# Kernel optimization log

Measured on AMD Instinct MI355X. Metric: run time of the kernel, lower is better.

The kernel has to match this reference:

```python
import jax, jax.numpy as jnp
import numpy as np


def _conv_relu(x, w, b):
    # keras Conv2D: NHWC input, HWIO kernel, VALID padding, stride 1, relu
    y = jax.lax.conv_general_dilated(
        x, w, window_strides=(1, 1), padding='VALID',
        dimension_numbers=('NHWC', 'HWIO', 'NHWC'))
    return jax.nn.relu(y + b)


def _maxpool2(x):
    # keras MaxPooling2D((2,2)): window 2x2, stride 2, VALID
    return jax.lax.reduce_window(
        x, -jnp.inf, jax.lax.max,
        window_dimensions=(1, 2, 2, 1), window_strides=(1, 2, 2, 1),
        padding='VALID')


def setup_inputs() -> dict:
    key = jax.random.key(0)
    ks = jax.random.split(key, 8)
    B = 4096
    return {
        'x': jax.random.normal(ks[0], (B, 14, 14, 1), jnp.float32),
        'conv1_w': jax.random.normal(ks[1], (3, 3, 1, 32), jnp.float32) * 0.1,
        'conv1_b': jnp.zeros((32,), jnp.float32),
        'conv2_w': jax.random.normal(ks[2], (3, 3, 32, 64), jnp.float32) * 0.05,
        'conv2_b': jnp.zeros((64,), jnp.float32),
        # trainable grid, initialized as tf.linspace(0,1,grid_size=50)
        'grid': jnp.linspace(0.0, 1.0, 50, dtype=jnp.float32),
        # KANLayer splines: output_dim=128 weights, each (input_dim=256, grid_size=50)
        'kan1_w': jax.random.normal(ks[3], (128, 256, 50), jnp.float32) * 0.05,
        # SimplifiedKANLayer splines: output_dim=64 weights, each (input_dim=128,)
        'kan2_w': jax.random.normal(ks[4], (64, 128), jnp.float32) * 0.05,
        'dense_w': jax.random.normal(ks[5], (64, 10), jnp.float32) * 0.05,
        'dense_b': jnp.zeros((10,), jnp.float32),
    }


def reference(x, conv1_w, conv1_b, conv2_w, conv2_b, grid, kan1_w, kan2_w,
              dense_w, dense_b):
    h = _conv_relu(x, conv1_w, conv1_b)   # (B,12,12,32)
    h = _maxpool2(h)                      # (B,6,6,32)
    h = _conv_relu(h, conv2_w, conv2_b)   # (B,4,4,64)
    h = _maxpool2(h)                      # (B,2,2,64)
    B = h.shape[0]
    h = h.reshape(B, -1)                  # (B,256) keras Flatten order (H,W,C)
    # KANLayer: linear hat basis relu(1-|x-g|) per (feature,grid), contracted
    # against per-output coefficients: out[b,o] = sum_{d,g} W[o,d,g]*basis[b,d,g]
    basis = jax.nn.relu(1.0 - jnp.abs(h[:, :, None] - grid[None, None, :]))  # (B,256,50)
    h = jnp.einsum('bdg,odg->bo', basis, kan1_w)  # (B,128)
    # SimplifiedKANLayer: out[b,o] = sum_d W2[o,d]*relu(h[b,d])
    h = jnp.einsum('bd,od->bo', jax.nn.relu(h), kan2_w)  # (B,64)
    return jax.nn.softmax(h @ dense_w + dense_b, axis=-1)  # (B,10)
```

## Files before the change

### kernel.cpp

```cpp
#include <hip/hip_runtime.h>
#include <hip/hip_bf16.h>
#include <hip/hip_fp16.h>

typedef float v2f __attribute__((ext_vector_type(2)));
typedef _Float16 f16x8 __attribute__((ext_vector_type(8)));
typedef float f32x4 __attribute__((ext_vector_type(4)));

__global__ __launch_bounds__(256) void k_prep(
    const float* __restrict__ kan1_w, const float* __restrict__ w2,
    const float* __restrict__ kan2_w, __half* __restrict__ tabN,
    _Float16* __restrict__ w2f, __half2* __restrict__ w2t) {
  __shared__ float wsh[128][51];
  int bid = blockIdx.x;
  int t = threadIdx.x;
  if (bid < 256) {
    int d = bid;
#pragma unroll
    for (int i = t; i < 128 * 50; i += 256) {
      int oo = i / 50;
      int g = i - oo * 50;
      wsh[oo][g] = kan1_w[(size_t)oo * 12800 + (size_t)d * 50 + g];
    }
    __syncthreads();
    int o = t & 127;
    int jh = t >> 7;
    const float* wr = &wsh[o][0];
    __half* trow = tabN + (size_t)d * 197 * 128 + o;
    const float inv98 = 1.0f / 98.0f;
    float lowW, lowG, highW, highG;
    int k0, k1;
    if (jh == 0) {
      lowW = wr[0]; lowG = 0.f; highW = 0.f; highG = 0.f;
      for (int g = 1; g < 50; ++g) {
        highW += wr[g];
        highG += wr[g] * ((float)g * (1.0f / 49.0f));
      }
      k0 = 0; k1 = 49;
    } else {
      lowW = 0.f; lowG = 0.f; highW = 0.f; highG = 0.f;
      for (int g = 1; g < 50; ++g) {
        lowW += wr[g];
        lowG += wr[g] * ((float)g * (1.0f / 49.0f));
      }
      k0 = 49; k1 = 98;
    }
    for (int k = k0; k < k1; ++k) {
      float A = highW - lowW;
      float Bc = (lowW + highW) + lowG - highG;
      float c0 = (float)(2 * k) * inv98 + 0.5f * inv98;
      float c1 = c0 + inv98;
      trow[(size_t)(2 * k) * 128] = __float2half(fmaf(A, c0, Bc));
      trow[(size_t)(2 * k + 1) * 128] = __float2half(fmaf(A, c1, Bc));
      if (k + 1 <= 49) {
        float wg = wr[k + 1], gg = (float)(k + 1) * (1.0f / 49.0f);
        lowW += wg; lowG += wg * gg;
        highW -= wg; highG -= wg * gg;
      }
      if (k >= 48) {
        float wg = wr[k - 48], gg = (float)(k - 48) * (1.0f / 49.0f);
        lowW -= wg; lowG -= wg * gg;
      }
    }
    if (jh == 1) trow[(size_t)196 * 128] = __float2half(0.f);
    return;
  }
  if (bid < 328) {
    int i = (bid - 256) * 256 + t;
    int n = i & 63;
    int row = i >> 6;
    int ci = row & 31;
    int tap = row >> 5;
    w2f[((tap * 4 + (ci >> 3)) * 64 + n) * 8 + (ci & 7)] = (_Float16)w2[i];
    return;
  }
  {
    int i = (bid - 328) * 256 + t;
    int dp = i >> 6;
    int o = i & 63;
    w2t[i] = __floats2half2_rn(kan2_w[o * 128 + 2 * dp],
                               kan2_w[o * 128 + 2 * dp + 1]);
  }
}

#define NBC 4

__global__ __launch_bounds__(256)
__attribute__((amdgpu_waves_per_eu(2, 4))) void k_main(
    const float* __restrict__ x, const float* __restrict__ w1,
    const float* __restrict__ b1, const _Float16* __restrict__ w2f,
    const float* __restrict__ b2, const __half* __restrict__ tabN,
    const __half2* __restrict__ w2t, const float* __restrict__ dense_w,
    const float* __restrict__ dense_b, float* __restrict__ out) {
  __shared__ __align__(16) char sm1[4864];
  __shared__ __align__(16) char sm2[11520];
  float* xs = (float*)sm1;
  float* w1s = xs + NBC * 224;
  float* b1s = w1s + 288;
  unsigned short* meta = (unsigned short*)sm1;
  _Float16* h1l = (_Float16*)sm2;
  float* vs = (float*)sm2;
  float* us = vs + NBC * 128;
  float* ls = us + NBC * 64;
  int t = threadIdx.x;
  int bid = blockIdx.x;
  int b0 = bid * NBC;
  {
    for (int i = t; i < NBC * 224; i += 256) {
      int blb = i / 224;
      int rem = i - blb * 224;
      int r = rem >> 4;
      int cc = rem & 15;
      xs[i] = (cc < 14) ? x[(size_t)(b0 + blb) * 196 + r * 14 + cc] : 0.f;
    }
    for (int i = t; i < 288; i += 256) w1s[i] = w1[i];
    if (t < 32) b1s[t] = b1[t];
  }
  __syncthreads();
  int p = t >> 6;
  int c = t & 63;
  {
    int ch = c & 31;
    int half = c >> 5;
    float wr[9];
#pragma unroll
    for (int j = 0; j < 9; ++j) wr[j] = w1s[j * 32 + ch];
    float bias = b1s[ch];
    int y0 = 3 * half;
    const float* xb = xs + p * 224;
    _Float16* hrow = h1l + p * 1440 + ch;
#pragma unroll
    for (int yy = 0; yy < 3; ++yy) {
      int y = y0 + yy;
      float xr[4][16];
#pragma unroll
      for (int r = 0; r < 4; ++r) {
        float4* dstp = (float4*)xr[r];
        const float4* srcp = (const float4*)(xb + (2 * y + r) * 16);
#pragma unroll
        for (int q = 0; q < 4; ++q) dstp[q] = srcp[q];
      }
#pragma unroll
      for (int xx = 0; xx < 6; ++xx) {
        float m = -1e30f;
#pragma unroll
        for (int py = 0; py < 2; ++py)
#pragma unroll
          for (int px = 0; px < 2; ++px) {
            float s = 0.f;
#pragma unroll
            for (int dy = 0; dy < 3; ++dy)
#pragma unroll
              for (int dx = 0; dx < 3; ++dx)
                s = fmaf(xr[py + dy][2 * xx + px + dx], wr[dy * 3 + dx], s);
            m = fmaxf(m, s);
          }
        hrow[(y * 6 + xx) * 40] = (_Float16)fmaxf(m + bias, 0.f);
      }
    }
  }
  __syncthreads();
  {
    int lm = c & 15;
    int lk = c >> 4;
    int mbase = (lm >> 2) * 6 + (lm & 3);
    f32x4 acc[4];
#pragma unroll
    for (int nt = 0; nt < 4; ++nt) acc[nt] = (f32x4){0.f, 0.f, 0.f, 0.f};
    const _Float16* h0 = &h1l[p * 1440 + lk * 8];
#pragma unroll
    for (int tap = 0; tap < 9; ++tap) {
      int tapoff = (tap / 3) * 6 + (tap % 3);
      int po = (mbase + tapoff) * 40;
      f16x8 a0 = *(const f16x8*)(h0 + po);
      const _Float16* wb = &w2f[((tap * 4 + lk) * 64 + lm) * 8];
      f16x8 bf0 = *(const f16x8*)(wb);
      f16x8 bf1 = *(const f16x8*)(wb + 128);
      f16x8 bf2 = *(const f16x8*)(wb + 256);
      f16x8 bf3 = *(const f16x8*)(wb + 384);
      acc[0] = __builtin_amdgcn_mfma_f32_16x16x32_f16(a0, bf0, acc[0], 0, 0, 0);
      acc[1] = __builtin_amdgcn_mfma_f32_16x16x32_f16(a0, bf1, acc[1], 0, 0, 0);
      acc[2] = __builtin_amdgcn_mfma_f32_16x16x32_f16(a0, bf2, acc[2], 0, 0, 0);
      acc[3] = __builtin_amdgcn_mfma_f32_16x16x32_f16(a0, bf3, acc[3], 0, 0, 0);
    }
    float bias[4];
#pragma unroll
    for (int nt = 0; nt < 4; ++nt) bias[nt] = b2[nt * 16 + lm];
#pragma unroll
    for (int nt = 0; nt < 4; ++nt) {
      f32x4 A = acc[nt];
      float m01 = fmaxf(A.x, A.y);
      float m23 = fmaxf(A.z, A.w);
      m01 = fmaxf(m01, __shfl_xor(m01, 16));
      m23 = fmaxf(m23, __shfl_xor(m23, 16));
      float val = (lk & 1) ? m23 : m01;
      val = fmaxf(val + bias[nt], 0.f);
      int d = lk * 64 + nt * 16 + lm;
      int k = (int)(val * 98.0f);
      k = k > 196 ? 196 : k;
      meta[d * NBC + p] = (unsigned short)(d * 197 + k);
    }
  }
  __syncthreads();
  {
    int lq = c >> 4;
    int lo = c & 15;
    int phase0 = bid & 7;
    v2f acc[4];
#pragma unroll
    for (int e = 0; e < 4; ++e) acc[e] = (v2f){0.f, 0.f};
    for (int ph = 0; ph < 8; ++ph) {
      int d0 = ((phase0 + ph) & 7) << 5;
      int offs[8];
#pragma unroll
      for (int dq = 0; dq < 8; ++dq)
        offs[dq] = ((int)meta[(d0 + 4 * dq + lq) * NBC + p]) << 7;
      float4 raws[8];
#pragma unroll
      for (int dq = 0; dq < 8; ++dq)
        raws[dq] = *(const float4*)(tabN + offs[dq] + lo * 8);
      __half2 hs[4];
#pragma unroll
      for (int e = 0; e < 4; ++e) hs[e] = __builtin_bit_cast(__half2, 0u);
#pragma unroll
      for (int dq = 0; dq < 8; ++dq) {
        hs[0] = __hadd2(hs[0], __builtin_bit_cast(__half2, raws[dq].x));
        hs[1] = __hadd2(hs[1], __builtin_bit_cast(__half2, raws[dq].y));
        hs[2] = __hadd2(hs[2], __builtin_bit_cast(__half2, raws[dq].z));
        hs[3] = __hadd2(hs[3], __builtin_bit_cast(__half2, raws[dq].w));
      }
#pragma unroll
      for (int e = 0; e < 4; ++e) {
        float2 f = __half22float2(hs[e]);
        acc[e].x += f.x;
        acc[e].y += f.y;
      }
    }
#pragma unroll
    for (int e = 0; e < 4; ++e) {
      acc[e].x += __shfl_xor(acc[e].x, 16);
      acc[e].y += __shfl_xor(acc[e].y, 16);
      acc[e].x += __shfl_xor(acc[e].x, 32);
      acc[e].y += __shfl_xor(acc[e].y, 32);
    }
    if (lq == 0) {
      float* vp = vs + p * 128 + lo * 8;
      *(float4*)vp = make_float4(fmaxf(acc[0].x, 0.f), fmaxf(acc[0].y, 0.f),
                                 fmaxf(acc[1].x, 0.f), fmaxf(acc[1].y, 0.f));
      *(float4*)(vp + 4) =
          make_float4(fmaxf(acc[2].x, 0.f), fmaxf(acc[2].y, 0.f),
                      fmaxf(acc[3].x, 0.f), fmaxf(acc[3].y, 0.f));
    }
  }
  __syncthreads();
  {
    float a = 0.f;
    const float* v0 = vs + p * 128;
#pragma unroll 8
    for (int dp = 0; dp < 64; ++dp) {
      float2 wf = __half22float2(w2t[dp * 64 + c]);
      float2 vq = *(const float2*)(v0 + 2 * dp);
      a = fmaf(wf.x, vq.x, a);
      a = fmaf(wf.y, vq.y, a);
    }
    us[p * 64 + c] = a;
  }
  __syncthreads();
  if (t < NBC * 10) {
    int b = t / 10;
    int j = t - b * 10;
    float s = dense_b[j];
    for (int k2 = 0; k2 < 64; ++k2)
      s = fmaf(us[b * 64 + k2], dense_w[k2 * 10 + j], s);
    ls[b * 12 + j] = s;
  }
  __syncthreads();
  if (t < NBC) {
    int b = t;
    float m = -1e30f;
#pragma unroll
    for (int j = 0; j < 10; ++j) m = fmaxf(m, ls[b * 12 + j]);
    float e[10];
    float sum = 0.f;
#pragma unroll
    for (int j = 0; j < 10; ++j) {
      e[j] = __expf(ls[b * 12 + j] - m);
      sum += e[j];
    }
    float inv = 1.0f / sum;
#pragma unroll
    for (int j = 0; j < 10; ++j) out[(size_t)(b0 + b) * 10 + j] = e[j] * inv;
  }
}

extern "C" void kernel_launch(void* const* d_in, const int* in_sizes, int n_in,
                              void* d_out, int out_size, void* d_ws, size_t ws_size,
                              hipStream_t stream) {
  const float* x      = (const float*)d_in[0];
  const float* w1     = (const float*)d_in[1];
  const float* b1     = (const float*)d_in[2];
  const float* w2     = (const float*)d_in[3];
  const float* b2     = (const float*)d_in[4];
  const float* kan1_w = (const float*)d_in[6];
  const float* kan2_w = (const float*)d_in[7];
  const float* dw     = (const float*)d_in[8];
  const float* db     = (const float*)d_in[9];
  float* out = (float*)d_out;
  int B = in_sizes[0] / 196;

  char* wsb = (char*)d_ws;
  __half* tabN = (__half*)wsb;
  size_t off1 = (size_t)256 * 197 * 128 * sizeof(__half);
  off1 = (off1 + 255) & ~(size_t)255;
  _Float16* w2f = (_Float16*)(wsb + off1);
  size_t off2 = off1 + 18432 * sizeof(_Float16);
  off2 = (off2 + 255) & ~(size_t)255;
  __half2* w2t = (__half2*)(wsb + off2);

  k_prep<<<dim3(344), dim3(256), 0, stream>>>(kan1_w, w2, kan2_w, tabN, w2f, w2t);
  k_main<<<dim3(B / NBC), dim3(256), 0, stream>>>(
      x, w1, b1, w2f, b2, tabN, w2t, dw, db, out);
}
```

Measured before the change: 110.8 us.

## Split KAN table prep across more blocks and double-buffer table gathers

The prep kernel now assigns four blocks per input feature, each thread computing one eighth of the 98 table segments with its own prefix-sum initialisation, so the serial per-thread loop is shorter and more blocks fill the GPU. The main kernel's KAN gather loop is fully unrolled and double-buffered, issuing the next phase's table loads before accumulating the current one to hide memory latency. The cost is four-fold redundant loading of weights into shared memory in prep and higher register pressure in the main kernel, which may reduce occupancy.

```diff
diff --git a/kernel.cpp b/kernel.cpp
--- a/kernel.cpp
+++ b/kernel.cpp
@@ -13,8 +13,9 @@
   __shared__ float wsh[128][51];
   int bid = blockIdx.x;
   int t = threadIdx.x;
-  if (bid < 256) {
-    int d = bid;
+  if (bid < 1024) {
+    int d = bid >> 2;
+    int q = bid & 3;
 #pragma unroll
     for (int i = t; i < 128 * 50; i += 256) {
       int oo = i / 50;
@@ -27,22 +28,21 @@
     const float* wr = &wsh[o][0];
     __half* trow = tabN + (size_t)d * 197 * 128 + o;
     const float inv98 = 1.0f / 98.0f;
-    float lowW, lowG, highW, highG;
-    int k0, k1;
-    if (jh == 0) {
-      lowW = wr[0]; lowG = 0.f; highW = 0.f; highG = 0.f;
-      for (int g = 1; g < 50; ++g) {
-        highW += wr[g];
-        highG += wr[g] * ((float)g * (1.0f / 49.0f));
-      }
-      k0 = 0; k1 = 49;
-    } else {
-      lowW = 0.f; lowG = 0.f; highW = 0.f; highG = 0.f;
-      for (int g = 1; g < 50; ++g) {
-        lowW += wr[g];
-        lowG += wr[g] * ((float)g * (1.0f / 49.0f));
-      }
-      k0 = 49; k1 = 98;
+    int ci = q * 2 + jh;
+    int k0 = (ci * 98) >> 3;
+    int k1 = ((ci + 1) * 98) >> 3;
+    float lowW = 0.f, lowG = 0.f, highW = 0.f, highG = 0.f;
+    {
+      int gl0 = k0 - 48 > 0 ? k0 - 48 : 0;
+      int gl1 = k0 < 49 ? k0 : 49;
+      for (int g = gl0; g <= gl1; ++g) {
+        float w = wr[g], gg = (float)g * (1.0f / 49.0f);
+        lowW += w; lowG += w * gg;
+      }
+      for (int g = k0 + 1; g < 50; ++g) {
+        float w = wr[g], gg = (float)g * (1.0f / 49.0f);
+        highW += w; highG += w * gg;
+      }
     }
     for (int k = k0; k < k1; ++k) {
       float A = highW - lowW;
@@ -61,11 +61,11 @@
         lowW -= wg; lowG -= wg * gg;
       }
     }
-    if (jh == 1) trow[(size_t)196 * 128] = __float2half(0.f);
+    if (ci == 7) trow[(size_t)196 * 128] = __float2half(0.f);
     return;
   }
-  if (bid < 328) {
-    int i = (bid - 256) * 256 + t;
+  if (bid < 1096) {
+    int i = (bid - 1024) * 256 + t;
     int n = i & 63;
     int row = i >> 6;
     int ci = row & 31;
@@ -74,7 +74,7 @@
     return;
   }
   {
-    int i = (bid - 328) * 256 + t;
+    int i = (bid - 1096) * 256 + t;
     int dp = i >> 6;
     int o = i & 63;
     w2t[i] = __floats2half2_rn(kan2_w[o * 128 + 2 * dp],
@@ -208,25 +208,38 @@
     v2f acc[4];
 #pragma unroll
     for (int e = 0; e < 4; ++e) acc[e] = (v2f){0.f, 0.f};
+    int offs[2][8];
+    float4 raws[2][8];
+    {
+      int d0 = (phase0 & 7) << 5;
+#pragma unroll
+      for (int dq = 0; dq < 8; ++dq)
+        offs[0][dq] = ((int)meta[(d0 + 4 * dq + lq) * NBC + p]) << 7;
+#pragma unroll
+      for (int dq = 0; dq < 8; ++dq)
+        raws[0][dq] = *(const float4*)(tabN + offs[0][dq] + lo * 8);
+    }
+#pragma unroll
     for (int ph = 0; ph < 8; ++ph) {
-      int d0 = ((phase0 + ph) & 7) << 5;
-      int offs[8];
-#pragma unroll
-      for (int dq = 0; dq < 8; ++dq)
-        offs[dq] = ((int)meta[(d0 + 4 * dq + lq) * NBC + p]) << 7;
-      float4 raws[8];
-#pragma unroll
-      for (int dq = 0; dq < 8; ++dq)
-        raws[dq] = *(const float4*)(tabN + offs[dq] + lo * 8);
+      const int cur = ph & 1, nxt = cur ^ 1;
+      if (ph < 7) {
+        int d0n = ((phase0 + ph + 1) & 7) << 5;
+#pragma unroll
+        for (int dq = 0; dq < 8; ++dq)
+          offs[nxt][dq] = ((int)meta[(d0n + 4 * dq + lq) * NBC + p]) << 7;
+#pragma unroll
+        for (int dq = 0; dq < 8; ++dq)
+          raws[nxt][dq] = *(const float4*)(tabN + offs[nxt][dq] + lo * 8);
+      }
       __half2 hs[4];
 #pragma unroll
       for (int e = 0; e < 4; ++e) hs[e] = __builtin_bit_cast(__half2, 0u);
 #pragma unroll
       for (int dq = 0; dq < 8; ++dq) {
-        hs[0] = __hadd2(hs[0], __builtin_bit_cast(__half2, raws[dq].x));
-        hs[1] = __hadd2(hs[1], __builtin_bit_cast(__half2, raws[dq].y));
-        hs[2] = __hadd2(hs[2], __builtin_bit_cast(__half2, raws[dq].z));
-        hs[3] = __hadd2(hs[3], __builtin_bit_cast(__half2, raws[dq].w));
+        hs[0] = __hadd2(hs[0], __builtin_bit_cast(__half2, raws[cur][dq].x));
+        hs[1] = __hadd2(hs[1], __builtin_bit_cast(__half2, raws[cur][dq].y));
+        hs[2] = __hadd2(hs[2], __builtin_bit_cast(__half2, raws[cur][dq].z));
+        hs[3] = __hadd2(hs[3], __builtin_bit_cast(__half2, raws[cur][dq].w));
       }
 #pragma unroll
       for (int e = 0; e < 4; ++e) {
@@ -316,7 +329,7 @@
   off2 = (off2 + 255) & ~(size_t)255;
   __half2* w2t = (__half2*)(wsb + off2);
 
-  k_prep<<<dim3(344), dim3(256), 0, stream>>>(kan1_w, w2, kan2_w, tabN, w2f, w2t);
+  k_prep<<<dim3(1112), dim3(256), 0, stream>>>(kan1_w, w2, kan2_w, tabN, w2f, w2t);
   k_main<<<dim3(B / NBC), dim3(256), 0, stream>>>(
       x, w1, b1, w2f, b2, tabN, w2t, dw, db, out);
 }
```

New measurement: 111.4 us. Within noise of the previous version (+0.6%).
